# Performance work log

Hardware: AMD Instinct MI355X
Metric: run time of the kernel (lower is better)

## Reference

```python
import jax, jax.numpy as jnp
import numpy as np

B = 2048      # batch
L = 128       # signal_length
PL = 8        # patch_length (nodes per graph)
PS = 4        # patch_stride
LW = 4        # local_window
P = (L - PL) // PS + 1   # num_patches = 31
H = 128       # gnn/rnn hidden dim
C = 8         # num_classes


def _mean_adj():
    # A[i, j] = 1/deg(i) for 0 < |i-j| <= LW; exact mean aggregation of SAGEConv
    A = np.zeros((PL, PL), np.float32)
    for i in range(PL):
        nb = [j for j in range(PL) if 0 < abs(i - j) <= LW]
        for j in nb:
            A[i, j] = 1.0 / len(nb)
    return jnp.asarray(A)


def setup_inputs() -> dict:
    key = jax.random.key(0)
    ks = jax.random.split(key, 10)
    def n(k, shape, s):
        return jax.random.normal(k, shape, dtype=jnp.float32) * s
    inp = {
        "iq_signal": jax.random.normal(ks[0], (B, 2, L), dtype=jnp.float32),
        # SAGE layer 0 (in=2 -> H): lin_l (neighbor, with bias), lin_r (root, no bias)
        "Wl0": n(ks[1], (H, 2), 0.3), "bl0": jnp.zeros((H,), jnp.float32), "Wr0": n(ks[2], (H, 2), 0.3),
        # SAGE layers 1-2 (H -> H), stacked
        "Wl12": n(ks[3], (2, H, H), 0.08), "bl12": jnp.zeros((2, H), jnp.float32), "Wr12": n(ks[4], (2, H, H), 0.08),
        # LayerNorm params for the 3 GNN layers
        "ln_gamma": jnp.ones((3, H), jnp.float32), "ln_beta": jnp.zeros((3, H), jnp.float32),
        # 2-layer GRU (input=H, hidden=H), PyTorch gate order [r, z, n]
        "gru_w_ih": n(ks[5], (2, 3 * H, H), 0.08), "gru_w_hh": n(ks[6], (2, 3 * H, H), 0.08),
        "gru_b_ih": jnp.zeros((2, 3 * H), jnp.float32), "gru_b_hh": jnp.zeros((2, 3 * H), jnp.float32),
    }
    # ETF matrix: sqrt(C/(C-1)) * Q @ (I - J/C), Q from QR of random [H, C]
    Pm = jax.random.normal(ks[7], (H, C), dtype=jnp.float32)
    Q, _ = jnp.linalg.qr(Pm)
    I = jnp.eye(C, dtype=jnp.float32)
    J = jnp.ones((C, C), jnp.float32)
    inp["etf"] = (np.float32(np.sqrt(C / (C - 1))) * (Q @ (I - J / C))).astype(jnp.float32)
    return inp


def _layernorm(h, g, b):
    mu = h.mean(-1, keepdims=True)
    var = h.var(-1, keepdims=True)
    return (h - mu) / jnp.sqrt(var + 1e-5) * g + b


def _gru_layer(seq, w_ih, w_hh, b_ih, b_hh):
    # seq: [B, T, H]; precompute input gates for all timesteps
    xg = jnp.einsum('bti,gi->btg', seq, w_ih) + b_ih  # [B, T, 3H]
    def step(hprev, xg_t):
        hg = hprev @ w_hh.T + b_hh
        r = jax.nn.sigmoid(xg_t[:, :H] + hg[:, :H])
        z = jax.nn.sigmoid(xg_t[:, H:2 * H] + hg[:, H:2 * H])
        nn_ = jnp.tanh(xg_t[:, 2 * H:] + r * hg[:, 2 * H:])
        hnew = (1.0 - z) * nn_ + z * hprev
        return hnew, hnew
    h0 = jnp.zeros((seq.shape[0], H), seq.dtype)
    _, outs = jax.lax.scan(step, h0, xg.transpose(1, 0, 2))
    return outs.transpose(1, 0, 2)  # [B, T, H]


def reference(iq_signal, Wl0, bl0, Wr0, Wl12, bl12, Wr12, ln_gamma, ln_beta,
              gru_w_ih, gru_w_hh, gru_b_ih, gru_b_hh, etf):
    # --- DTSG: patch extraction -> [B*P, PL, 2] node features ---
    starts = jnp.arange(P) * PS
    idx = starts[:, None] + jnp.arange(PL)[None, :]       # [P, PL]
    x = iq_signal[:, :, idx]                              # [B, 2, P, PL]
    x = x.transpose(0, 2, 3, 1).reshape(B * P, PL, 2)     # [G, 8, 2]

    A = _mean_adj()  # identical graph for every patch; dense mean-aggregation

    def sage(h, Wl, bl, Wr):
        agg = jnp.einsum('ij,gjf->gif', A, h)             # mean neighbor aggregation
        return jnp.einsum('gif,of->gio', agg, Wl) + bl + jnp.einsum('gif,of->gio', h, Wr)

    # PatchGNN (dropout = identity in eval); edge_attr is ignored by PyG SAGEConv
    h = jax.nn.relu(_layernorm(sage(x, Wl0, bl0, Wr0), ln_gamma[0], ln_beta[0]))
    for i in range(2):
        hn = jax.nn.relu(_layernorm(sage(h, Wl12[i], bl12[i], Wr12[i]), ln_gamma[i + 1], ln_beta[i + 1]))
        h = h + hn  # residual (shapes match for layers 1,2)

    patch_features = h.mean(axis=1)                       # global_mean_pool -> [B*P, H]

    # --- TemporalRNN: 2-layer GRU, take last timestep ---
    seq = patch_features.reshape(B, P, H)
    o = _gru_layer(seq, gru_w_ih[0], gru_w_hh[0], gru_b_ih[0], gru_b_hh[0])
    o = _gru_layer(o, gru_w_ih[1], gru_w_hh[1], gru_b_ih[1], gru_b_hh[1])
    g = o[:, -1, :]                                       # [B, H]

    logits_g = g @ etf                                    # [B, C]
    return logits_g, g, patch_features
```

## Files before the change

kernel.cpp:

```cpp
#include <hip/hip_runtime.h>
#include <hip/hip_bf16.h>

typedef __attribute__((ext_vector_type(8))) short bf16x8;
typedef __attribute__((ext_vector_type(4))) float f32x4;

__device__ __forceinline__ unsigned short f2bf(float v) {
    union { __hip_bfloat16 h; unsigned short u; } cv;
    cv.h = __float2bfloat16(v);
    return cv.u;
}
__device__ __forceinline__ float bf2f(unsigned short u) {
    return __uint_as_float(((unsigned int)u) << 16);
}
__device__ __forceinline__ float sigm(float x) { return 1.f / (1.f + __expf(-x)); }
__device__ __forceinline__ float tanh_(float x) { return 2.f / (1.f + __expf(-2.f * x)) - 1.f; }
__device__ __forceinline__ float adjW(int i, int j) {
    const float inv[8] = {1.f/4.f, 1.f/5.f, 1.f/6.f, 1.f/7.f,
                          1.f/7.f, 1.f/6.f, 1.f/5.f, 1.f/4.f};
    int d = i - j; d = d < 0 ? -d : d;
    return (d >= 1 && d <= 4) ? inv[i] : 0.f;
}

template<int CTRL>
__device__ __forceinline__ float dppadd(float v) {
    int d = __builtin_amdgcn_update_dpp(0, __float_as_int(v), CTRL, 0xF, 0xF, true);
    return v + __int_as_float(d);
}
__device__ __forceinline__ float rowsum16(float v) {
    v = dppadd<0xB1>(v);
    v = dppadd<0x4E>(v);
    v = dppadd<0x124>(v);
    v = dppadd<0x128>(v);
    return v;
}

__global__ __launch_bounds__(256) void k0_wconv(const float* __restrict__ Wl12,
    const float* __restrict__ Wr12, const float* __restrict__ wih,
    const float* __restrict__ whh, const float* __restrict__ Wl0,
    const float* __restrict__ Wr0, unsigned short* __restrict__ wbf)
{
    int i = blockIdx.x * 256 + threadIdx.x;
    if (i < 262144) {
        float v; int base, j;
        if (i < 32768)        { v = Wl12[i];        base = (i >> 14) * 16384;           j = i & 16383; }
        else if (i < 65536)   { int s = i - 32768;  v = Wr12[s]; base = 32768 + (s >> 14) * 16384; j = s & 16383; }
        else if (i < 163840)  { int s = i - 65536;  v = wih[s];  base = 65536 + (s / 49152) * 49152; j = s % 49152; }
        else                  { int s = i - 163840; v = whh[s];  base = 163840 + (s / 49152) * 49152; j = s % 49152; }
        int col = j >> 7, k = j & 127;
        int perm = ((col >> 4) * 4 + (k >> 5)) * 512 + ((k >> 3) & 3) * 128 + (col & 15) * 8 + (k & 7);
        wbf[base + perm] = f2bf(v);
    } else {
        int e2 = i - 262144;
        int ct  = e2 >> 9;
        int off = e2 & 511;
        int li2 = off >> 7;
        int rem = off & 127;
        int colLow = rem >> 3;
        int kLow = off & 7;
        int k = li2 * 8 + kLow;
        int col = ct * 16 + colLow;
        float v = 0.f;
        if (k < 2)      v = Wl0[col * 2 + k];
        else if (k < 4) v = Wr0[col * 2 + k - 2];
        wbf[i] = f2bf(v);
    }
}

__global__ __launch_bounds__(256, 4) void k1_sage(
    const float* __restrict__ iq,
    const float* __restrict__ bl0,
    const unsigned short* __restrict__ wbf,
    const float* __restrict__ bl12,
    const float* __restrict__ lng, const float* __restrict__ lnb,
    float* __restrict__ pf)
{
    __shared__ unsigned short hT[64 * 128];
    __shared__ float statS[64][4];
    __shared__ float xS[64][2], axS[64][2];

    const int t  = threadIdx.x;
    const int l  = t & 63;
    const int w  = t >> 6;
    const int wr = w >> 1, wc = w & 1;
    const int lc = l & 15, li = l >> 4;
    const int kgrp = li * 8;
    const int half = li & 1;
    const int g0 = blockIdx.x * 8;

    if (t < 128) {
        int r = t >> 1, c = t & 1;
        int gid = g0 + (r >> 3);
        int node = r & 7;
        int b = gid / 31, p = gid - b * 31;
        xS[r][c] = iq[((size_t)b * 2 + c) * 128 + p * 4 + node];
    }
    __syncthreads();
    if (t < 128) {
        int r = t >> 1, c = t & 1;
        int node = r & 7, base = r & ~7;
        float s = 0.f;
        #pragma unroll
        for (int j = 0; j < 8; ++j) s += adjW(node, j) * xS[base + j][c];
        axS[r][c] = s;
    }
    __syncthreads();

    f32x4 acc[2][4];

    auto ln_epi = [&](const float* gptr, const float* btptr, bool resid) {
        float rs[2][4], rq[2][4];
        #pragma unroll
        for (int mt = 0; mt < 2; ++mt) {
            f32x4 sv = (acc[mt][0] + acc[mt][1]) + (acc[mt][2] + acc[mt][3]);
            f32x4 qv = acc[mt][0] * acc[mt][0] + acc[mt][1] * acc[mt][1]
                     + acc[mt][2] * acc[mt][2] + acc[mt][3] * acc[mt][3];
            #pragma unroll
            for (int q = 0; q < 4; ++q) {
                rs[mt][q] = rowsum16(sv[q]);
                rq[mt][q] = rowsum16(qv[q]);
            }
        }
        if (lc == 0) {
            #pragma unroll
            for (int mt = 0; mt < 2; ++mt)
                #pragma unroll
                for (int q = 0; q < 4; ++q) {
                    int row = wr * 32 + mt * 16 + li * 4 + q;
                    statS[row][wc * 2]     = rs[mt][q];
                    statS[row][wc * 2 + 1] = rq[mt][q];
                }
        }
        __syncthreads();
        float gam[4], bet[4];
        #pragma unroll
        for (int nt = 0; nt < 4; ++nt) {
            int col = wc * 64 + nt * 16 + lc;
            gam[nt] = gptr[col]; bet[nt] = btptr[col];
        }
        #pragma unroll
        for (int mt = 0; mt < 2; ++mt)
            #pragma unroll
            for (int q = 0; q < 4; ++q) {
                int row = wr * 32 + mt * 16 + li * 4 + q;
                int s8 = (row & 7) << 3;
                float4 st = *(const float4*)&statS[row][0];
                float sum = st.x + st.z, sq = st.y + st.w;
                float mu   = sum * (1.f / 128.f);
                float var  = sq * (1.f / 128.f) - mu * mu;
                float rstd = rsqrtf(var + 1e-5f);
                #pragma unroll
                for (int nt = 0; nt < 4; ++nt) {
                    int col = wc * 64 + nt * 16 + lc;
                    int idx = row * 128 + (col ^ s8);
                    float ag = rstd * gam[nt];
                    float bg = __builtin_fmaf(-mu, ag, bet[nt]);
                    float v  = fmaxf(__builtin_fmaf(acc[mt][nt][q], ag, bg), 0.f);
                    float hn = resid ? (bf2f(hT[idx]) + v) : v;
                    hT[idx] = f2bf(hn);
                }
            }
        __syncthreads();
    };

    {
        bf16x8 xA[2];
        #pragma unroll
        for (int mt = 0; mt < 2; ++mt) {
            bf16x8 v = (bf16x8){0, 0, 0, 0, 0, 0, 0, 0};
            if (li == 0) {
                int row = wr * 32 + mt * 16 + lc;
                v[0] = (short)f2bf(axS[row][0]); v[1] = (short)f2bf(axS[row][1]);
                v[2] = (short)f2bf(xS[row][0]);  v[3] = (short)f2bf(xS[row][1]);
            }
            xA[mt] = v;
        }
        const unsigned short* w0f = wbf + 262144;
        #pragma unroll
        for (int nt = 0; nt < 4; ++nt) {
            float bv = bl0[wc * 64 + nt * 16 + lc];
            acc[0][nt] = (f32x4){bv, bv, bv, bv};
            acc[1][nt] = (f32x4){bv, bv, bv, bv};
        }
        #pragma unroll
        for (int nt = 0; nt < 4; ++nt) {
            bf16x8 b0 = *(const bf16x8*)&w0f[(wc * 4 + nt) * 512 + l * 8];
            acc[0][nt] = __builtin_amdgcn_mfma_f32_16x16x32_bf16(xA[0], b0, acc[0][nt], 0, 0, 0);
            acc[1][nt] = __builtin_amdgcn_mfma_f32_16x16x32_bf16(xA[1], b0, acc[1][nt], 0, 0, 0);
        }
        ln_epi(lng, lnb, false);
    }

    const int aswz = (lc & 7) << 3;
    #pragma unroll 1
    for (int lay = 0; lay < 2; ++lay) {
        bf16x8 hA[2][4];
        #pragma unroll
        for (int mt = 0; mt < 2; ++mt)
            #pragma unroll
            for (int ks = 0; ks < 4; ++ks) {
                int row = wr * 32 + 16 * mt + lc;
                hA[mt][ks] = *(const bf16x8*)&hT[row * 128 + ((ks * 32 + kgrp) ^ aswz)];
            }

        const unsigned short* wl  = wbf + lay * 16384;
        const unsigned short* wrp = wbf + 32768 + lay * 16384;

        #pragma unroll
        for (int nt = 0; nt < 4; ++nt) {
            float bv = bl12[lay * 128 + wc * 64 + nt * 16 + lc];
            acc[0][nt] = (f32x4){bv, bv, bv, bv};
            acc[1][nt] = (f32x4){bv, bv, bv, bv};
        }

        #pragma unroll
        for (int ks = 0; ks < 4; ++ks) {
            #pragma unroll
            for (int nt = 0; nt < 4; ++nt) {
                bf16x8 b = *(const bf16x8*)&wl[((wc * 4 + nt) * 4 + ks) * 512 + l * 8];
                acc[0][nt] = __builtin_amdgcn_mfma_f32_16x16x32_bf16(hA[0][ks], b, acc[0][nt], 0, 0, 0);
                acc[1][nt] = __builtin_amdgcn_mfma_f32_16x16x32_bf16(hA[1][ks], b, acc[1][nt], 0, 0, 0);
            }
        }

        #pragma unroll
        for (int mt = 0; mt < 2; ++mt)
            #pragma unroll
            for (int nt = 0; nt < 4; ++nt) {
                float own[4], oth[4];
                #pragma unroll
                for (int q = 0; q < 4; ++q) {
                    own[q] = acc[mt][nt][q];
                    oth[q] = __shfl_xor(own[q], 16, 64);
                }
                float yL[4], yH[4];
                #pragma unroll
                for (int q = 0; q < 4; ++q) {
                    yL[q] = half ? oth[q] : own[q];
                    yH[q] = half ? own[q] : oth[q];
                }
                float S = yL[0]+yL[1]+yL[2]+yL[3]+yH[0]+yH[1]+yH[2]+yH[3];
                float o0, o1, o2, o3;
                if (!half) {
                    o0 = (S - yL[0] - yH[1] - yH[2] - yH[3]) * 0.25f;
                    o1 = (S - yL[1] - yH[2] - yH[3]) * 0.2f;
                    o2 = (S - yL[2] - yH[3]) * (1.f/6.f);
                    o3 = (S - yL[3]) * (1.f/7.f);
                } else {
                    o0 = (S - yH[0]) * (1.f/7.f);
                    o1 = (S - yH[1] - yL[0]) * (1.f/6.f);
                    o2 = (S - yH[2] - yL[0] - yL[1]) * 0.2f;
                    o3 = (S - yH[3] - yL[0] - yL[1] - yL[2]) * 0.25f;
                }
                acc[mt][nt][0] = o0; acc[mt][nt][1] = o1;
                acc[mt][nt][2] = o2; acc[mt][nt][3] = o3;
            }

        #pragma unroll
        for (int ks = 0; ks < 4; ++ks) {
            #pragma unroll
            for (int nt = 0; nt < 4; ++nt) {
                bf16x8 b = *(const bf16x8*)&wrp[((wc * 4 + nt) * 4 + ks) * 512 + l * 8];
                acc[0][nt] = __builtin_amdgcn_mfma_f32_16x16x32_bf16(hA[0][ks], b, acc[0][nt], 0, 0, 0);
                acc[1][nt] = __builtin_amdgcn_mfma_f32_16x16x32_bf16(hA[1][ks], b, acc[1][nt], 0, 0, 0);
            }
        }

        ln_epi(lng + (lay + 1) * 128, lnb + (lay + 1) * 128, true);
    }

    {
        const int gi = t >> 5, c0 = t & 31;
        #pragma unroll
        for (int k = 0; k < 4; ++k) {
            int c = c0 + 32 * k;
            float s = 0.f;
            #pragma unroll
            for (int j = 0; j < 8; ++j)
                s += bf2f(hT[(gi * 8 + j) * 128 + (c ^ (j << 3))]);
            pf[(size_t)(g0 + gi) * 128 + c] = s * 0.125f;
        }
    }
}

__global__ __launch_bounds__(256) void k2_xg(
    const float* __restrict__ src, const unsigned short* __restrict__ wB,
    const float* __restrict__ bias, unsigned short* __restrict__ out)
{
    const int t = threadIdx.x, w = t >> 6, l = t & 63;
    const int lc = l & 15, li = l >> 4;
    const int m0 = blockIdx.x * 64 + w * 16;

    bf16x8 aA[4];
    #pragma unroll
    for (int ks = 0; ks < 4; ++ks) {
        const float* p = src + (size_t)(m0 + lc) * 128 + ks * 32 + li * 8;
        float4 f0 = *(const float4*)p;
        float4 f1 = *(const float4*)(p + 4);
        bf16x8 v;
        v[0] = (short)f2bf(f0.x); v[1] = (short)f2bf(f0.y);
        v[2] = (short)f2bf(f0.z); v[3] = (short)f2bf(f0.w);
        v[4] = (short)f2bf(f1.x); v[5] = (short)f2bf(f1.y);
        v[6] = (short)f2bf(f1.z); v[7] = (short)f2bf(f1.w);
        aA[ks] = v;
    }
    #pragma unroll 2
    for (int nt = 0; nt < 24; ++nt) {
        float bv = bias[nt * 16 + lc];
        f32x4 acc = (f32x4){bv, bv, bv, bv};
        #pragma unroll
        for (int ks = 0; ks < 4; ++ks) {
            bf16x8 b = *(const bf16x8*)&wB[(size_t)(nt * 4 + ks) * 512 + l * 8];
            acc = __builtin_amdgcn_mfma_f32_16x16x32_bf16(aA[ks], b, acc, 0, 0, 0);
        }
        #pragma unroll
        for (int q = 0; q < 4; ++q) {
            int m = m0 + li * 4 + q;
            out[(size_t)m * 384 + nt * 16 + lc] = f2bf(acc[q]);
        }
    }
}

__global__ __launch_bounds__(512, 2) void k3_gru(
    const unsigned short* __restrict__ xg, const unsigned short* __restrict__ wbf,
    const float* __restrict__ bih, const float* __restrict__ bhh,
    const float* __restrict__ etf,
    float* __restrict__ gbuf, float* __restrict__ logits)
{
    __shared__ unsigned short h1S[16][136];
    __shared__ unsigned short h2S[16][136];

    const int t = threadIdx.x, w = t >> 6, l = t & 63;
    const int lc = l & 15, li = l >> 4;
    const int col = w * 16 + lc;
    const int kgrp = li * 8;
    const int b0 = blockIdx.x * 8;
    const bool act = (li < 2);

    for (int i = t; i < 16 * 136; i += 512) {
        ((unsigned short*)h1S)[i] = 0;
        ((unsigned short*)h2S)[i] = 0;
    }

    const unsigned short* wih2 = wbf + 114688;
    const unsigned short* whh1 = wbf + 163840;
    const unsigned short* whh2 = wbf + 212992;
    bf16x8 Wh1[3][4], Wi2[3][4], Wh2[3][4];
    #pragma unroll
    for (int g = 0; g < 3; ++g)
        #pragma unroll
        for (int ks = 0; ks < 4; ++ks) {
            size_t off = (size_t)((g * 8 + w) * 4 + ks) * 512 + l * 8;
            Wh1[g][ks] = *(const bf16x8*)(whh1 + off);
            Wi2[g][ks] = *(const bf16x8*)(wih2 + off);
            Wh2[g][ks] = *(const bf16x8*)(whh2 + off);
        }
    float bh1[3], bi2[3], bh2[3];
    #pragma unroll
    for (int g = 0; g < 3; ++g) {
        bh1[g] = bhh[g * 128 + col];
        bi2[g] = bih[384 + g * 128 + col];
        bh2[g] = bhh[384 + g * 128 + col];
    }

    float h1r[4] = {0.f, 0.f, 0.f, 0.f};
    float h2r[4] = {0.f, 0.f, 0.f, 0.f};
    float x1[3][4];

    if (act) {
        #pragma unroll
        for (int g = 0; g < 3; ++g)
            #pragma unroll
            for (int q = 0; q < 4; ++q)
                x1[g][q] = bf2f(xg[((size_t)(b0 + li * 4 + q) * 31 + 0) * 384 + g * 128 + col]);
    }
    __syncthreads();

    for (int ts = 0; ts < 31; ++ts) {
        bf16x8 aH[4];
        #pragma unroll
        for (int ks = 0; ks < 4; ++ks) aH[ks] = *(const bf16x8*)&h1S[lc][ks * 32 + kgrp];
        f32x4 acc[3];
        #pragma unroll
        for (int g = 0; g < 3; ++g) {
            acc[g] = (f32x4){0.f, 0.f, 0.f, 0.f};
            #pragma unroll
            for (int ks = 0; ks < 4; ++ks)
                acc[g] = __builtin_amdgcn_mfma_f32_16x16x32_bf16(aH[ks], Wh1[g][ks], acc[g], 0, 0, 0);
        }
        float xn[3][4];
        if (act && ts < 30) {
            #pragma unroll
            for (int g = 0; g < 3; ++g)
                #pragma unroll
                for (int q = 0; q < 4; ++q)
                    xn[g][q] = bf2f(xg[((size_t)(b0 + li * 4 + q) * 31 + ts + 1) * 384 + g * 128 + col]);
        }
        if (act) {
            #pragma unroll
            for (int q = 0; q < 4; ++q) {
                float r  = sigm(x1[0][q] + acc[0][q] + bh1[0]);
                float z  = sigm(x1[1][q] + acc[1][q] + bh1[1]);
                float nn = tanh_(x1[2][q] + r * (acc[2][q] + bh1[2]));
                h1r[q] = (1.f - z) * nn + z * h1r[q];
            }
        }
        __syncthreads();
        if (act) {
            #pragma unroll
            for (int q = 0; q < 4; ++q) h1S[li * 4 + q][col] = f2bf(h1r[q]);
        }
        __syncthreads();

        bf16x8 aH1n[4], aH2[4];
        #pragma unroll
        for (int ks = 0; ks < 4; ++ks) {
            aH1n[ks] = *(const bf16x8*)&h1S[lc][ks * 32 + kgrp];
            aH2[ks]  = *(const bf16x8*)&h2S[lc][ks * 32 + kgrp];
        }
        f32x4 ax2[3], ah2[3];
        #pragma unroll
        for (int g = 0; g < 3; ++g) {
            ax2[g] = (f32x4){0.f, 0.f, 0.f, 0.f};
            ah2[g] = (f32x4){0.f, 0.f, 0.f, 0.f};
            #pragma unroll
            for (int ks = 0; ks < 4; ++ks) {
                ax2[g] = __builtin_amdgcn_mfma_f32_16x16x32_bf16(aH1n[ks], Wi2[g][ks], ax2[g], 0, 0, 0);
                ah2[g] = __builtin_amdgcn_mfma_f32_16x16x32_bf16(aH2[ks],  Wh2[g][ks], ah2[g], 0, 0, 0);
            }
        }
        if (act) {
            #pragma unroll
            for (int q = 0; q < 4; ++q) {
                float xr = ax2[0][q] + bi2[0];
                float xz = ax2[1][q] + bi2[1];
                float xn2 = ax2[2][q] + bi2[2];
                float r  = sigm(xr + ah2[0][q] + bh2[0]);
                float z  = sigm(xz + ah2[1][q] + bh2[1]);
                float nn = tanh_(xn2 + r * (ah2[2][q] + bh2[2]));
                h2r[q] = (1.f - z) * nn + z * h2r[q];
            }
        }
        __syncthreads();
        if (act) {
            #pragma unroll
            for (int q = 0; q < 4; ++q) h2S[li * 4 + q][col] = f2bf(h2r[q]);
        }
        __syncthreads();

        #pragma unroll
        for (int g = 0; g < 3; ++g)
            #pragma unroll
            for (int q = 0; q < 4; ++q) x1[g][q] = xn[g][q];
    }

    if (act) {
        #pragma unroll
        for (int q = 0; q < 4; ++q)
            gbuf[(size_t)(b0 + li * 4 + q) * 128 + col] = h2r[q];
    }

    float* fS = (float*)&h1S[0][0];
    __syncthreads();
    if (act) {
        #pragma unroll
        for (int q = 0; q < 4; ++q) fS[(li * 4 + q) * 128 + col] = h2r[q];
    }
    __syncthreads();
    if (t < 64) {
        int row = t >> 3, c = t & 7;
        float s = 0.f;
        #pragma unroll 8
        for (int f = 0; f < 128; ++f) s += fS[row * 128 + f] * etf[f * 8 + c];
        logits[(size_t)(b0 + row) * 8 + c] = s;
    }
}

extern "C" void kernel_launch(void* const* d_in, const int* in_sizes, int n_in,
                              void* d_out, int out_size, void* d_ws, size_t ws_size,
                              hipStream_t stream) {
    const float* iq   = (const float*)d_in[0];
    const float* Wl0  = (const float*)d_in[1];
    const float* bl0  = (const float*)d_in[2];
    const float* Wr0  = (const float*)d_in[3];
    const float* Wl12 = (const float*)d_in[4];
    const float* bl12 = (const float*)d_in[5];
    const float* Wr12 = (const float*)d_in[6];
    const float* lng  = (const float*)d_in[7];
    const float* lnb  = (const float*)d_in[8];
    const float* wih  = (const float*)d_in[9];
    const float* whh  = (const float*)d_in[10];
    const float* bih  = (const float*)d_in[11];
    const float* bhh  = (const float*)d_in[12];
    const float* etf  = (const float*)d_in[13];

    float* out    = (float*)d_out;
    float* logits = out;
    float* gbuf   = out + 16384;
    float* pf     = out + 16384 + 262144;

    unsigned short* wbf = (unsigned short*)d_ws;
    unsigned short* xg  = wbf + 266240;

    k0_wconv<<<1040, 256, 0, stream>>>(Wl12, Wr12, wih, whh, Wl0, Wr0, wbf);
    k1_sage<<<7936, 256, 0, stream>>>(iq, bl0, wbf, bl12, lng, lnb, pf);
    k2_xg<<<992, 256, 0, stream>>>(pf, wbf + 65536, bih, xg);
    k3_gru<<<256, 512, 0, stream>>>(xg, wbf, bih, bhh, etf, gbuf, logits);
}
```

Measured before the change: 305.3 us.

## Fuse layer-1 GRU input projection into SAGE kernel and double-buffer GRU hidden state

Measured after the change: 325.6 us. 1.07x slower.

```diff
diff --git a/kernel.cpp b/kernel.cpp
--- a/kernel.cpp
+++ b/kernel.cpp
@@ -72,7 +72,8 @@
     const unsigned short* __restrict__ wbf,
     const float* __restrict__ bl12,
     const float* __restrict__ lng, const float* __restrict__ lnb,
-    float* __restrict__ pf)
+    const float* __restrict__ bih,
+    float* __restrict__ pf, unsigned short* __restrict__ xg)
 {
     __shared__ unsigned short hT[64 * 128];
     __shared__ float statS[64][4];
@@ -268,6 +269,7 @@
         ln_epi(lng + (lay + 1) * 128, lnb + (lay + 1) * 128, true);
     }
 
+    float sv[4];
     {
         const int gi = t >> 5, c0 = t & 31;
         #pragma unroll
@@ -277,45 +279,44 @@
             #pragma unroll
             for (int j = 0; j < 8; ++j)
                 s += bf2f(hT[(gi * 8 + j) * 128 + (c ^ (j << 3))]);
-            pf[(size_t)(g0 + gi) * 128 + c] = s * 0.125f;
-        }
-    }
-}
-
-__global__ __launch_bounds__(256) void k2_xg(
-    const float* __restrict__ src, const unsigned short* __restrict__ wB,
-    const float* __restrict__ bias, unsigned short* __restrict__ out)
-{
-    const int t = threadIdx.x, w = t >> 6, l = t & 63;
-    const int lc = l & 15, li = l >> 4;
-    const int m0 = blockIdx.x * 64 + w * 16;
-
-    bf16x8 aA[4];
-    #pragma unroll
-    for (int ks = 0; ks < 4; ++ks) {
-        const float* p = src + (size_t)(m0 + lc) * 128 + ks * 32 + li * 8;
-        float4 f0 = *(const float4*)p;
-        float4 f1 = *(const float4*)(p + 4);
-        bf16x8 v;
-        v[0] = (short)f2bf(f0.x); v[1] = (short)f2bf(f0.y);
-        v[2] = (short)f2bf(f0.z); v[3] = (short)f2bf(f0.w);
-        v[4] = (short)f2bf(f1.x); v[5] = (short)f2bf(f1.y);
-        v[6] = (short)f2bf(f1.z); v[7] = (short)f2bf(f1.w);
-        aA[ks] = v;
-    }
-    #pragma unroll 2
-    for (int nt = 0; nt < 24; ++nt) {
-        float bv = bias[nt * 16 + lc];
-        f32x4 acc = (f32x4){bv, bv, bv, bv};
-        #pragma unroll
-        for (int ks = 0; ks < 4; ++ks) {
-            bf16x8 b = *(const bf16x8*)&wB[(size_t)(nt * 4 + ks) * 512 + l * 8];
-            acc = __builtin_amdgcn_mfma_f32_16x16x32_bf16(aA[ks], b, acc, 0, 0, 0);
-        }
-        #pragma unroll
-        for (int q = 0; q < 4; ++q) {
-            int m = m0 + li * 4 + q;
-            out[(size_t)m * 384 + nt * 16 + lc] = f2bf(acc[q]);
+            sv[k] = s * 0.125f;
+            pf[(size_t)(g0 + gi) * 128 + c] = sv[k];
+        }
+    }
+    __syncthreads();
+    {
+        const int gi = t >> 5, c0 = t & 31;
+        #pragma unroll
+        for (int k = 0; k < 4; ++k) {
+            int c = c0 + 32 * k;
+            hT[gi * 128 + (c ^ (gi << 3))] = f2bf(sv[k]);
+        }
+    }
+    __syncthreads();
+
+    {
+        bf16x8 aA[4];
+        #pragma unroll
+        for (int ks = 0; ks < 4; ++ks)
+            aA[ks] = *(const bf16x8*)&hT[lc * 128 + ((ks * 32 + kgrp) ^ ((lc & 7) << 3))];
+        const unsigned short* wih1 = wbf + 65536;
+        #pragma unroll
+        for (int j = 0; j < 6; ++j) {
+            int ct = w * 6 + j;
+            float bv = bih[ct * 16 + lc];
+            f32x4 a = (f32x4){bv, bv, bv, bv};
+            #pragma unroll
+            for (int ks = 0; ks < 4; ++ks) {
+                bf16x8 b = *(const bf16x8*)&wih1[(ct * 4 + ks) * 512 + l * 8];
+                a = __builtin_amdgcn_mfma_f32_16x16x32_bf16(aA[ks], b, a, 0, 0, 0);
+            }
+            if (li < 2) {
+                #pragma unroll
+                for (int q = 0; q < 4; ++q) {
+                    int m = g0 + li * 4 + q;
+                    xg[(size_t)m * 384 + ct * 16 + lc] = f2bf(a[q]);
+                }
+            }
         }
     }
 }
@@ -326,8 +327,8 @@
     const float* __restrict__ etf,
     float* __restrict__ gbuf, float* __restrict__ logits)
 {
-    __shared__ unsigned short h1S[16][136];
-    __shared__ unsigned short h2S[16][136];
+    __shared__ unsigned short h1S[2][16][136];
+    __shared__ unsigned short h2S[2][16][136];
 
     const int t = threadIdx.x, w = t >> 6, l = t & 63;
     const int lc = l & 15, li = l >> 4;
@@ -336,7 +337,7 @@
     const int b0 = blockIdx.x * 8;
     const bool act = (li < 2);
 
-    for (int i = t; i < 16 * 136; i += 512) {
+    for (int i = t; i < 2 * 16 * 136; i += 512) {
         ((unsigned short*)h1S)[i] = 0;
         ((unsigned short*)h2S)[i] = 0;
     }
@@ -375,10 +376,12 @@
     }
     __syncthreads();
 
+    int cur = 0;
     for (int ts = 0; ts < 31; ++ts) {
+        const int nxt = cur ^ 1;
         bf16x8 aH[4];
         #pragma unroll
-        for (int ks = 0; ks < 4; ++ks) aH[ks] = *(const bf16x8*)&h1S[lc][ks * 32 + kgrp];
+        for (int ks = 0; ks < 4; ++ks) aH[ks] = *(const bf16x8*)&h1S[cur][lc][ks * 32 + kgrp];
         f32x4 acc[3];
         #pragma unroll
         for (int g = 0; g < 3; ++g) {
@@ -403,19 +406,16 @@
                 float nn = tanh_(x1[2][q] + r * (acc[2][q] + bh1[2]));
                 h1r[q] = (1.f - z) * nn + z * h1r[q];
             }
+            #pragma unroll
+            for (int q = 0; q < 4; ++q) h1S[nxt][li * 4 + q][col] = f2bf(h1r[q]);
         }
         __syncthreads();
-        if (act) {
-            #pragma unroll
-            for (int q = 0; q < 4; ++q) h1S[li * 4 + q][col] = f2bf(h1r[q]);
-        }
-        __syncthreads();
 
         bf16x8 aH1n[4], aH2[4];
         #pragma unroll
         for (int ks = 0; ks < 4; ++ks) {
-            aH1n[ks] = *(const bf16x8*)&h1S[lc][ks * 32 + kgrp];
-            aH2[ks]  = *(const bf16x8*)&h2S[lc][ks * 32 + kgrp];
+            aH1n[ks] = *(const bf16x8*)&h1S[nxt][lc][ks * 32 + kgrp];
+            aH2[ks]  = *(const bf16x8*)&h2S[cur][lc][ks * 32 + kgrp];
         }
         f32x4 ax2[3], ah2[3];
         #pragma unroll
@@ -431,26 +431,24 @@
         if (act) {
             #pragma unroll
             for (int q = 0; q < 4; ++q) {
-                float xr = ax2[0][q] + bi2[0];
-                float xz = ax2[1][q] + bi2[1];
+                float xr  = ax2[0][q] + bi2[0];
+                float xz  = ax2[1][q] + bi2[1];
                 float xn2 = ax2[2][q] + bi2[2];
                 float r  = sigm(xr + ah2[0][q] + bh2[0]);
                 float z  = sigm(xz + ah2[1][q] + bh2[1]);
                 float nn = tanh_(xn2 + r * (ah2[2][q] + bh2[2]));
                 h2r[q] = (1.f - z) * nn + z * h2r[q];
             }
+            #pragma unroll
+            for (int q = 0; q < 4; ++q) h2S[nxt][li * 4 + q][col] = f2bf(h2r[q]);
         }
         __syncthreads();
-        if (act) {
-            #pragma unroll
-            for (int q = 0; q < 4; ++q) h2S[li * 4 + q][col] = f2bf(h2r[q]);
-        }
-        __syncthreads();
 
         #pragma unroll
         for (int g = 0; g < 3; ++g)
             #pragma unroll
             for (int q = 0; q < 4; ++q) x1[g][q] = xn[g][q];
+        cur = nxt;
     }
 
     if (act) {
@@ -459,7 +457,7 @@
             gbuf[(size_t)(b0 + li * 4 + q) * 128 + col] = h2r[q];
     }
 
-    float* fS = (float*)&h1S[0][0];
+    float* fS = (float*)&h1S[0][0][0];
     __syncthreads();
     if (act) {
         #pragma unroll
@@ -502,7 +500,6 @@
     unsigned short* xg  = wbf + 266240;
 
     k0_wconv<<<1040, 256, 0, stream>>>(Wl12, Wr12, wih, whh, Wl0, Wr0, wbf);
-    k1_sage<<<7936, 256, 0, stream>>>(iq, bl0, wbf, bl12, lng, lnb, pf);
-    k2_xg<<<992, 256, 0, stream>>>(pf, wbf + 65536, bih, xg);
+    k1_sage<<<7936, 256, 0, stream>>>(iq, bl0, wbf, bl12, lng, lnb, bih, pf, xg);
     k3_gru<<<256, 512, 0, stream>>>(xg, wbf, bih, bhh, etf, gbuf, logits);
 }
```

## Double-buffer GRU hidden states in LDS and retile xg for coalesced loads

Applied to the files above, without the earlier changes.

Result: no change. 307.0 us, median of 2 (+0.5%).

```diff
diff --git a/kernel.cpp b/kernel.cpp
--- a/kernel.cpp
+++ b/kernel.cpp
@@ -304,18 +304,18 @@
         aA[ks] = v;
     }
     #pragma unroll 2
-    for (int nt = 0; nt < 24; ++nt) {
-        float bv = bias[nt * 16 + lc];
+    for (int ct = 0; ct < 24; ++ct) {
+        float bv = bias[ct * 16 + lc];
         f32x4 acc = (f32x4){bv, bv, bv, bv};
         #pragma unroll
         for (int ks = 0; ks < 4; ++ks) {
-            bf16x8 b = *(const bf16x8*)&wB[(size_t)(nt * 4 + ks) * 512 + l * 8];
+            bf16x8 b = *(const bf16x8*)&wB[(size_t)(ct * 4 + ks) * 512 + l * 8];
             acc = __builtin_amdgcn_mfma_f32_16x16x32_bf16(aA[ks], b, acc, 0, 0, 0);
         }
         #pragma unroll
         for (int q = 0; q < 4; ++q) {
             int m = m0 + li * 4 + q;
-            out[(size_t)m * 384 + nt * 16 + lc] = f2bf(acc[q]);
+            out[((size_t)ct * 63488 + m) * 16 + lc] = f2bf(acc[q]);
         }
     }
 }
@@ -326,8 +326,8 @@
     const float* __restrict__ etf,
     float* __restrict__ gbuf, float* __restrict__ logits)
 {
-    __shared__ unsigned short h1S[16][136];
-    __shared__ unsigned short h2S[16][136];
+    __shared__ unsigned short h1S[2][16][136];
+    __shared__ unsigned short h2S[2][16][136];
 
     const int t = threadIdx.x, w = t >> 6, l = t & 63;
     const int lc = l & 15, li = l >> 4;
@@ -336,7 +336,7 @@
     const int b0 = blockIdx.x * 8;
     const bool act = (li < 2);
 
-    for (int i = t; i < 16 * 136; i += 512) {
+    for (int i = t; i < 2 * 16 * 136; i += 512) {
         ((unsigned short*)h1S)[i] = 0;
         ((unsigned short*)h2S)[i] = 0;
     }
@@ -366,19 +366,26 @@
     float h2r[4] = {0.f, 0.f, 0.f, 0.f};
     float x1[3][4];
 
+    auto xgld = [&](int g, int q, int ts) -> float {
+        size_t m = (size_t)(b0 + li * 4 + q) * 31 + ts;
+        return bf2f(xg[((size_t)(g * 8 + w) * 63488 + m) * 16 + lc]);
+    };
+
     if (act) {
         #pragma unroll
         for (int g = 0; g < 3; ++g)
             #pragma unroll
             for (int q = 0; q < 4; ++q)
-                x1[g][q] = bf2f(xg[((size_t)(b0 + li * 4 + q) * 31 + 0) * 384 + g * 128 + col]);
+                x1[g][q] = xgld(g, q, 0);
     }
     __syncthreads();
 
+    int cur = 0;
     for (int ts = 0; ts < 31; ++ts) {
+        const int nxt = cur ^ 1;
         bf16x8 aH[4];
         #pragma unroll
-        for (int ks = 0; ks < 4; ++ks) aH[ks] = *(const bf16x8*)&h1S[lc][ks * 32 + kgrp];
+        for (int ks = 0; ks < 4; ++ks) aH[ks] = *(const bf16x8*)&h1S[cur][lc][ks * 32 + kgrp];
         f32x4 acc[3];
         #pragma unroll
         for (int g = 0; g < 3; ++g) {
@@ -393,7 +400,7 @@
             for (int g = 0; g < 3; ++g)
                 #pragma unroll
                 for (int q = 0; q < 4; ++q)
-                    xn[g][q] = bf2f(xg[((size_t)(b0 + li * 4 + q) * 31 + ts + 1) * 384 + g * 128 + col]);
+                    xn[g][q] = xgld(g, q, ts + 1);
         }
         if (act) {
             #pragma unroll
@@ -403,19 +410,16 @@
                 float nn = tanh_(x1[2][q] + r * (acc[2][q] + bh1[2]));
                 h1r[q] = (1.f - z) * nn + z * h1r[q];
             }
+            #pragma unroll
+            for (int q = 0; q < 4; ++q) h1S[nxt][li * 4 + q][col] = f2bf(h1r[q]);
         }
         __syncthreads();
-        if (act) {
-            #pragma unroll
-            for (int q = 0; q < 4; ++q) h1S[li * 4 + q][col] = f2bf(h1r[q]);
-        }
-        __syncthreads();
 
         bf16x8 aH1n[4], aH2[4];
         #pragma unroll
         for (int ks = 0; ks < 4; ++ks) {
-            aH1n[ks] = *(const bf16x8*)&h1S[lc][ks * 32 + kgrp];
-            aH2[ks]  = *(const bf16x8*)&h2S[lc][ks * 32 + kgrp];
+            aH1n[ks] = *(const bf16x8*)&h1S[nxt][lc][ks * 32 + kgrp];
+            aH2[ks]  = *(const bf16x8*)&h2S[cur][lc][ks * 32 + kgrp];
         }
         f32x4 ax2[3], ah2[3];
         #pragma unroll
@@ -431,26 +435,24 @@
         if (act) {
             #pragma unroll
             for (int q = 0; q < 4; ++q) {
-                float xr = ax2[0][q] + bi2[0];
-                float xz = ax2[1][q] + bi2[1];
+                float xr  = ax2[0][q] + bi2[0];
+                float xz  = ax2[1][q] + bi2[1];
                 float xn2 = ax2[2][q] + bi2[2];
                 float r  = sigm(xr + ah2[0][q] + bh2[0]);
                 float z  = sigm(xz + ah2[1][q] + bh2[1]);
                 float nn = tanh_(xn2 + r * (ah2[2][q] + bh2[2]));
                 h2r[q] = (1.f - z) * nn + z * h2r[q];
             }
+            #pragma unroll
+            for (int q = 0; q < 4; ++q) h2S[nxt][li * 4 + q][col] = f2bf(h2r[q]);
         }
         __syncthreads();
-        if (act) {
-            #pragma unroll
-            for (int q = 0; q < 4; ++q) h2S[li * 4 + q][col] = f2bf(h2r[q]);
-        }
-        __syncthreads();
 
         #pragma unroll
         for (int g = 0; g < 3; ++g)
             #pragma unroll
             for (int q = 0; q < 4; ++q) x1[g][q] = xn[g][q];
+        cur = nxt;
     }
 
     if (act) {
@@ -459,7 +461,7 @@
             gbuf[(size_t)(b0 + li * 4 + q) * 128 + col] = h2r[q];
     }
 
-    float* fS = (float*)&h1S[0][0];
+    float* fS = (float*)&h1S[0][0][0];
     __syncthreads();
     if (act) {
         #pragma unroll
```
